# Kernel optimization log

Measured on AMD Instinct MI355X. Metric: run time of the kernel, lower is better.

## Reference

```python
import jax, jax.numpy as jnp
import numpy as np

NBATCH, NUMATOM, NEIGH = 16, 512, 48
NPAIR = NUMATOM * NEIGH
NTYPE, NWAVE, NIPSIN = 4, 8, 3
CUTOFF = 5.0  # note: cutoff_cosine is never applied in the original forward


def setup_inputs() -> dict:
    key = jax.random.key(0)
    k1, k2, k3, k4 = jax.random.split(key, 4)
    coordinates = jax.random.normal(k1, (NBATCH, NUMATOM, 3), jnp.float32) * 3.0
    numatoms = jnp.full((NBATCH, 1), NUMATOM, dtype=jnp.int32)  # unused by forward math
    atom_index = jax.random.randint(k2, (NBATCH, 2, NPAIR), 0, NUMATOM)
    shifts = jax.random.normal(k3, (NBATCH, NPAIR, 3), jnp.float32)  # all > -1e9 -> all pairs valid
    species = jax.random.randint(k4, (NBATCH * NUMATOM,), 0, NTYPE)
    rs = jnp.tile(jnp.linspace(0.5, 4.0, NWAVE, dtype=jnp.float32), (NTYPE, 1))
    inta = jnp.full((NTYPE, NWAVE), 0.1, dtype=jnp.float32)
    return {"coordinates": coordinates, "numatoms": numatoms, "atom_index": atom_index,
            "shifts": shifts, "species": species, "rs": rs, "inta": inta}


def _forward(coordinates, atom_index, shifts, species, rs, inta):
    nbatch, numatom, _ = coordinates.shape
    totnatom = nbatch * numatom
    npair = atom_index.shape[2]
    coords = coordinates.reshape(-1, 3)                      # (totnatom, 3)
    # (nbatch, 2, P) -> (2, nbatch*P) with per-molecule global offsets
    ai = atom_index.transpose(1, 0, 2).reshape(2, -1)
    offs = jnp.repeat(jnp.arange(nbatch) * numatom, npair)
    idx12 = ai + offs[None, :]
    sh = shifts.reshape(-1, 3)
    valid = jnp.all(sh > -1e9, axis=1)                       # padding mask (all True here)
    dist_vec = coords[idx12[0]] - coords[idx12[1]] + sh      # (N, 3)
    distances = jnp.linalg.norm(dist_vec, axis=-1)           # (N,)
    neigh_sp = species[idx12[0]]                             # (N,)
    # radial: exp(-10*inta_t*(r - rs_t)^2), species-gathered params
    g = jnp.exp(-10.0 * inta[neigh_sp] * jnp.square(distances[:, None] - rs[neigh_sp]))  # (N, nwave)
    # angular: repeated outer products of the unit direction vector
    u = (dist_vec / distances[:, None]).T                    # (3, N)
    parts, orb = [], jnp.ones((1, u.shape[1]), u.dtype)
    for _ in range(1, NIPSIN):
        orb = jnp.einsum('jn,kn->jkn', orb, u).reshape(-1, u.shape[1])
        parts.append(orb)
    angular = jnp.concatenate(parts, axis=0)                 # (len_index=12, N)
    index_para = jnp.concatenate([jnp.full((3 ** i,), i - 1, dtype=jnp.int32)
                                  for i in range(1, NIPSIN)])
    # outer product of angular and radial basis per pair
    oa = jnp.einsum('jn,nk->njk', angular, g)                # (N, len_index, nwave)
    density_cols = []
    for itype in range(NTYPE):
        m = ((neigh_sp == itype) & valid).astype(oa.dtype)
        pd = jax.ops.segment_sum(oa * m[:, None, None], idx12[0], num_segments=totnatom)
        pd = jnp.square(pd)                                  # (totnatom, len_index, nwave)
        # sum angular components of equal order (index_para); row NIPSIN-1 stays zero, as in torch
        idens = jax.ops.segment_sum(pd.transpose(1, 0, 2), index_para, num_segments=NIPSIN)
        density_cols.append(idens.transpose(1, 0, 2).reshape(totnatom, -1))
    density = jnp.stack(density_cols, axis=1)                # (totnatom, ntype, nipsin*nwave)
    return density.reshape(totnatom, -1)


def reference(coordinates, numatoms, atom_index, shifts, species, rs, inta):
    return _forward(coordinates, atom_index, shifts, species, rs, inta)
```

## Files before the change

### kernel.cpp

```cpp
#include <hip/hip_runtime.h>

#define NBATCH   16
#define NUMATOM  512
#define NEIGH    48
#define NPAIR    (NUMATOM * NEIGH)
#define TOTNATOM (NBATCH * NUMATOM)
#define NTYPE    4
#define NWAVE    8
#define OUT_PER_ATOM 96

#define APB   8
#define GPB   (NUMATOM / APB)
#define CAP   96

__global__ __launch_bounds__(512, 4) void fused_density(
        const float* __restrict__ coords,
        const int*   __restrict__ atom_index,
        const float* __restrict__ shifts,
        const int*   __restrict__ species,
        const float* __restrict__ rs,
        const float* __restrict__ inta,
        float*       __restrict__ out) {
    __shared__ float  lc[NUMATOM * 3];
    __shared__ int    dq[APB * CAP];
    __shared__ float4 pq[APB * CAP];
    __shared__ int    qn[APB];
    __shared__ int    lsp[APB];
    __shared__ float  lrs[NTYPE * NWAVE];
    __shared__ float  lia[NTYPE * NWAVE];

    int blk = blockIdx.x;
    int b   = blk >> 6;
    int g   = blk & (GPB - 1);
    int t   = threadIdx.x;
    int lo  = g * APB;

    const float* cb = coords + (size_t)b * NUMATOM * 3;
    for (int i = t; i < NUMATOM * 3; i += 512) lc[i] = cb[i];
    if (t < NTYPE * NWAVE) { lrs[t] = rs[t]; lia[t] = -10.0f * inta[t]; }
    if (t < APB) { qn[t] = 0; lsp[t] = species[b * NUMATOM + lo + t]; }
    __syncthreads();

    const int*   i0row = atom_index + ((size_t)b * 2 + 0) * NPAIR;
    const int*   i1row = atom_index + ((size_t)b * 2 + 1) * NPAIR;
    const float* shrow = shifts + (size_t)b * NPAIR * 3;

#pragma unroll 4
    for (int p = t; p < NPAIR; p += 512) {
        int a0 = i0row[p];
        if ((a0 >> 3) == g) {
            int al = a0 & (APB - 1);
            int s  = atomicAdd(&qn[al], 1);
            if (s < CAP) dq[al * CAP + s] = p;
        }
    }
    __syncthreads();

    int wv = t >> 6;
    int l  = t & 63;
    int c  = qn[wv]; if (c > CAP) c = CAP;

    int ga0 = 3 * (lo + wv);
    for (int k = l; k < c; k += 64) {
        int p  = dq[wv * CAP + k];
        int a1 = i1row[p];
        float dx = lc[ga0 + 0] - lc[3 * a1 + 0] + shrow[3 * p + 0];
        float dy = lc[ga0 + 1] - lc[3 * a1 + 1] + shrow[3 * p + 1];
        float dz = lc[ga0 + 2] - lc[3 * a1 + 2] + shrow[3 * p + 2];
        float r   = sqrtf(dx * dx + dy * dy + dz * dz);
        float inv = 1.0f / r;
        pq[wv * CAP + k] = make_float4(dx * inv, dy * inv, dz * inv, r);
    }
    __syncthreads();

    int sp = lsp[wv];
    int j  = l >> 3, w = l & 7;
    float rw = lrs[sp * NWAVE + w];
    float cw = lia[sp * NWAVE + w];

    int ia, ib;
    if (j < 3)       { ia = j;     ib = 3;     }
    else if (j < 6)  { ia = j - 3; ib = j - 3; }
    else if (j == 6) { ia = 0;     ib = 1;     }
    else             { ia = 0;     ib = 2;     }

    const float4* q = pq + wv * CAP;
    float acc = 0.0f, acc2 = 0.0f;
    int k = 0;
    for (; k + 4 <= c; k += 4) {
        float4 v0 = q[k];
        float4 v1 = q[k + 1];
        float4 v2 = q[k + 2];
        float4 v3 = q[k + 3];
        float d0 = v0.w - rw, d1 = v1.w - rw, d2 = v2.w - rw, d3 = v3.w - rw;
        float g0 = __expf(cw * d0 * d0);
        float g1 = __expf(cw * d1 * d1);
        float g2 = __expf(cw * d2 * d2);
        float g3 = __expf(cw * d3 * d3);
        float ua0 = (ia == 0) ? v0.x : (ia == 1) ? v0.y : v0.z;
        float ub0 = (ib == 0) ? v0.x : (ib == 1) ? v0.y : (ib == 2) ? v0.z : 1.0f;
        float ua1 = (ia == 0) ? v1.x : (ia == 1) ? v1.y : v1.z;
        float ub1 = (ib == 0) ? v1.x : (ib == 1) ? v1.y : (ib == 2) ? v1.z : 1.0f;
        float ua2 = (ia == 0) ? v2.x : (ia == 1) ? v2.y : v2.z;
        float ub2 = (ib == 0) ? v2.x : (ib == 1) ? v2.y : (ib == 2) ? v2.z : 1.0f;
        float ua3 = (ia == 0) ? v3.x : (ia == 1) ? v3.y : v3.z;
        float ub3 = (ib == 0) ? v3.x : (ib == 1) ? v3.y : (ib == 2) ? v3.z : 1.0f;
        acc  += ua0 * ub0 * g0 + ua1 * ub1 * g1
              + ua2 * ub2 * g2 + ua3 * ub3 * g3;
        acc2 += v0.y * v0.z * g0 + v1.y * v1.z * g1
              + v2.y * v2.z * g2 + v3.y * v3.z * g3;
    }
    for (; k < c; ++k) {
        float4 v = q[k];
        float d = v.w - rw;
        float gg = __expf(cw * d * d);
        float ua = (ia == 0) ? v.x : (ia == 1) ? v.y : v.z;
        float ub = (ib == 0) ? v.x : (ib == 1) ? v.y : (ib == 2) ? v.z : 1.0f;
        acc  += ua * ub * gg;
        acc2 += v.y * v.z * gg;
    }

    float dens = acc * acc;
    float A = (j < 3) ? dens : 0.0f;
    float B = (j >= 3 && j < 6) ? dens
            : (j >= 6) ? 2.0f * dens : 0.0f;
    if (l < 8) B = 2.0f * acc2 * acc2;

#pragma unroll
    for (int m = 8; m < 64; m <<= 1) {
        A += __shfl_xor(A, m);
        B += __shfl_xor(B, m);
    }

    int a = (b << 9) + lo + wv;
    float* ob = out + (size_t)a * OUT_PER_ATOM;
    {
        int o = l, ity = o / 24, rem = o % 24, od = rem >> 3;
        ob[o] = (ity == sp && od < 2) ? (od == 0 ? A : B) : 0.0f;
    }
    if (l < 32) {
        int o = l + 64, ity = o / 24, rem = o % 24, od = rem >> 3;
        ob[o] = (ity == sp && od < 2) ? (od == 0 ? A : B) : 0.0f;
    }
}


extern "C" void kernel_launch(void* const* d_in, const int* in_sizes, int n_in,
                              void* d_out, int out_size, void* d_ws, size_t ws_size,
                              hipStream_t stream) {
    const float* coords     = (const float*)d_in[0];
    const int*   atom_index = (const int*)  d_in[2];
    const float* shifts     = (const float*)d_in[3];
    const int*   species    = (const int*)  d_in[4];
    const float* rs         = (const float*)d_in[5];
    const float* inta       = (const float*)d_in[6];
    float*       out        = (float*)      d_out;

    fused_density<<<NBATCH * GPB, 512, 0, stream>>>(
        coords, atom_index, shifts, species, rs, inta, out);
}
```

Baseline: 100.8 us.

## Pre-bucket pairs by atom group in a separate kernel instead of full scans

Adds a bucketing kernel that reads each molecule's first atom-index row once and appends each pair, packed with its local atom slot, to a per-group global bucket using global atomics. The density kernel then reads only its own bucket rather than every block scanning all pairs of its molecule. This removes the redundant per-block scan of the index array. In exchange it adds a memset, a second kernel launch, global atomic traffic and workspace use, and it caps each bucket at a fixed size.

```diff
diff --git a/kernel.cpp b/kernel.cpp
--- a/kernel.cpp
+++ b/kernel.cpp
@@ -9,9 +9,35 @@
 #define NWAVE    8
 #define OUT_PER_ATOM 96
 
-#define APB   8
-#define GPB   (NUMATOM / APB)
-#define CAP   96
+#define APB    8
+#define GPB    (NUMATOM / APB)
+#define NGRP   (NBATCH * GPB)
+#define CAP    96
+#define GCAP   512
+#define NCHUNK 12
+
+__global__ __launch_bounds__(512) void bucket_pairs(
+        const int* __restrict__ atom_index,
+        int*       __restrict__ gcnt,
+        int*       __restrict__ gbucket) {
+    int blk = blockIdx.x;
+    int b   = blk / NCHUNK;
+    int ch  = blk - b * NCHUNK;
+    int t   = threadIdx.x;
+
+    const int* i0row = atom_index + ((size_t)b * 2 + 0) * NPAIR + ch * 2048;
+
+#pragma unroll
+    for (int k = 0; k < 4; ++k) {
+        int i  = t + k * 512;
+        int p  = ch * 2048 + i;
+        int a0 = i0row[i];
+        int gid  = b * GPB + (a0 >> 3);
+        int slot = atomicAdd(&gcnt[gid], 1);
+        if (slot < GCAP)
+            gbucket[(size_t)gid * GCAP + slot] = p | ((a0 & (APB - 1)) << 16);
+    }
+}
 
 __global__ __launch_bounds__(512, 4) void fused_density(
         const float* __restrict__ coords,
@@ -20,6 +46,8 @@
         const int*   __restrict__ species,
         const float* __restrict__ rs,
         const float* __restrict__ inta,
+        const int*   __restrict__ gcnt,
+        const int*   __restrict__ gbucket,
         float*       __restrict__ out) {
     __shared__ float  lc[NUMATOM * 3];
     __shared__ int    dq[APB * CAP];
@@ -41,24 +69,22 @@
     if (t < APB) { qn[t] = 0; lsp[t] = species[b * NUMATOM + lo + t]; }
     __syncthreads();
 
-    const int*   i0row = atom_index + ((size_t)b * 2 + 0) * NPAIR;
-    const int*   i1row = atom_index + ((size_t)b * 2 + 1) * NPAIR;
-    const float* shrow = shifts + (size_t)b * NPAIR * 3;
-
-#pragma unroll 4
-    for (int p = t; p < NPAIR; p += 512) {
-        int a0 = i0row[p];
-        if ((a0 >> 3) == g) {
-            int al = a0 & (APB - 1);
-            int s  = atomicAdd(&qn[al], 1);
-            if (s < CAP) dq[al * CAP + s] = p;
-        }
+    int n = gcnt[blk]; if (n > GCAP) n = GCAP;
+    const int* gb = gbucket + (size_t)blk * GCAP;
+    for (int i = t; i < n; i += 512) {
+        int e  = gb[i];
+        int al = e >> 16;
+        int s  = atomicAdd(&qn[al], 1);
+        if (s < CAP) dq[al * CAP + s] = e & 0xFFFF;
     }
     __syncthreads();
 
     int wv = t >> 6;
     int l  = t & 63;
     int c  = qn[wv]; if (c > CAP) c = CAP;
+
+    const int*   i1row = atom_index + ((size_t)b * 2 + 1) * NPAIR;
+    const float* shrow = shifts + (size_t)b * NPAIR * 3;
 
     int ga0 = 3 * (lo + wv);
     for (int k = l; k < c; k += 64) {
@@ -156,6 +182,15 @@
     const float* inta       = (const float*)d_in[6];
     float*       out        = (float*)      d_out;
 
-    fused_density<<<NBATCH * GPB, 512, 0, stream>>>(
-        coords, atom_index, shifts, species, rs, inta, out);
+    const size_t cnt_bytes = (size_t)NGRP * sizeof(int);
+    const size_t gb_off    = (cnt_bytes + 255) & ~(size_t)255;
+    int* gcnt    = (int*)d_ws;
+    int* gbucket = (int*)((char*)d_ws + gb_off);
+
+    hipMemsetAsync(gcnt, 0, cnt_bytes, stream);
+
+    bucket_pairs<<<NBATCH * NCHUNK, 512, 0, stream>>>(atom_index, gcnt, gbucket);
+
+    fused_density<<<NGRP, 512, 0, stream>>>(
+        coords, atom_index, shifts, species, rs, inta, gcnt, gbucket, out);
 }
```

Result: slower. 131.8 us (+30.7%).
